# Kernel optimization log

Measured on AMD Instinct MI355X. Metric: run time of the kernel, lower is better.

The kernel has to match this reference:

```python
import jax, jax.numpy as jnp
import numpy as np

E = 256; H = 8; HD = E // H
L_LEN = 300; A_LEN = 250
T = 768; B = 4
NEG = -1e9


def setup_inputs() -> dict:
    rng = jax.random.key(0)
    ks = jax.random.split(rng, 16)
    n = lambda k, s, sc=1.0: jax.random.normal(k, s, dtype=jnp.float32) * sc
    return {
        "query": n(ks[0], (T, B, E)),
        "key": n(ks[1], (T, B, E)),
        "value": n(ks[2], (T, B, E)),
        "in_proj_w": n(ks[3], (3 * E, E), 0.05),
        "in_proj_b": jnp.zeros((3 * E,), jnp.float32),
        "out_w": n(ks[4], (7, E, E), 0.05),
        "out_b": jnp.zeros((7, E), jnp.float32),
        "s_l_w": n(ks[5], (E, 4 * E), 0.05),
        "s_l_b": jnp.zeros((E,), jnp.float32),
        "s_a_w": n(ks[6], (E, 4 * E), 0.05),
        "s_a_b": jnp.zeros((E,), jnp.float32),
        "s_v_w": n(ks[7], (E, 4 * E), 0.05),
        "s_v_b": jnp.zeros((E,), jnp.float32),
        "final_w": n(ks[8], (E, E), 0.05),
        "final_b": jnp.zeros((E,), jnp.float32),
    }


def _forward(query, key, value, in_proj_w, in_proj_b, out_w, out_b,
             s_l_w, s_l_b, s_a_w, s_a_b, s_v_w, s_v_b, final_w, final_b):
    t, b, e = query.shape
    scaling = HD ** -0.5
    Wq, Wk, Wv = in_proj_w[:E], in_proj_w[E:2 * E], in_proj_w[2 * E:]
    bq, bk, bv = in_proj_b[:E], in_proj_b[E:2 * E], in_proj_b[2 * E:]
    q = (query @ Wq.T + bq) * scaling
    k = key @ Wk.T + bk
    v = value @ Wv.T + bv
    # (T, B, E) -> (B*H, T, HD)
    sh = lambda x: x.reshape(t, b * H, HD).transpose(1, 0, 2)
    q, k, v = sh(q), sh(k), sh(v)
    # shared QK^T, reused by all 7 masked branches
    scores = jnp.einsum('bth,bsh->bts', q, k)  # (B*H, T, T)
    idx = jnp.arange(t)
    seg = jnp.where(idx < L_LEN, 0, jnp.where(idx < L_LEN + A_LEN, 1, 2))

    def branch(i, mods):
        # m[j] = 1 iff position j belongs to one of the selected modalities
        m = sum((seg == s) for s in mods).astype(scores.dtype)  # (T,)
        # additive mask: in-set query attends only in-set keys; out-of-set
        # query rows get all -1e9 (uniform softmax, zeroed by row mask below)
        add = jnp.where((m[:, None] * m[None, :]) > 0, 0.0, NEG)
        w = jax.nn.softmax(scores + add, axis=-1) * m[None, :, None]
        o = jnp.einsum('bts,bsh->bth', w, v * m[None, :, None])
        o = o.transpose(1, 0, 2).reshape(t, b, e)
        return o @ out_w[i].T + out_b[i]

    attn_lav = branch(0, (0, 1, 2))
    attn_la = branch(1, (0, 1))
    attn_lv = branch(2, (0, 2))
    attn_av = branch(3, (1, 2))
    attn_l = branch(4, (0,))
    attn_a = branch(5, (1,))
    attn_v = branch(6, (2,))

    sl = jnp.concatenate([attn_lav, attn_la, attn_lv, attn_l], -1) @ s_l_w.T + s_l_b
    sa = jnp.concatenate([attn_lav, attn_la, attn_av, attn_a], -1) @ s_a_w.T + s_a_b
    sv = jnp.concatenate([attn_lav, attn_lv, attn_av, attn_v], -1) @ s_v_w.T + s_v_b
    return (sl + sa + sv) @ final_w.T + final_b


def reference(query, key, value, in_proj_w, in_proj_b, out_w, out_b,
              s_l_w, s_l_b, s_a_w, s_a_b, s_v_w, s_v_b, final_w, final_b):
    return _forward(query, key, value, in_proj_w, in_proj_b, out_w, out_b,
                    s_l_w, s_l_b, s_a_w, s_a_b, s_v_w, s_v_b, final_w, final_b)
```

## Files before the change

### kernel.cpp

```cpp
#include <hip/hip_runtime.h>
#include <hip/hip_bf16.h>

#define E 256
#define H 8
#define HD 32
#define T 768
#define B 4
#define BH 32

typedef __attribute__((ext_vector_type(8))) short bf16x8;
typedef __attribute__((ext_vector_type(4))) float f32x4;
typedef __attribute__((ext_vector_type(16))) float f32x16;

__device__ __forceinline__ float b2f(__hip_bfloat16 x) { return __bfloat162float(x); }

__device__ __forceinline__ unsigned short f2bf_u(float x) {
    __hip_bfloat16 h = __float2bfloat16(x);
    return *(unsigned short*)&h;
}
__device__ __forceinline__ float bfu2f(unsigned short u) {
    return __uint_as_float(((unsigned int)u) << 16);
}

__device__ __forceinline__ int detect_f32(const void* query) {
    const unsigned short* q = (const unsigned short*)query;
    int lane = threadIdx.x & 63;
    int bad = 0;
    #pragma unroll
    for (int i = 0; i < 4; ++i) {
        float v = bfu2f(q[lane + i * 64]);
        bad |= (!(v == v) || fabsf(v) > 1e4f) ? 1 : 0;
    }
    return __any(bad) ? 1 : 0;
}

__device__ __forceinline__ void f8_split(const float* v, bf16x8& h, bf16x8& l) {
    #pragma unroll
    for (int e = 0; e < 8; ++e) {
        unsigned short hu = f2bf_u(v[e]);
        h[e] = (short)hu;
        l[e] = (short)f2bf_u(v[e] - bfu2f(hu));
    }
}

#define MFMA3(ACC, AH, AL, BH_, BL_)                                         \
    ACC = __builtin_amdgcn_mfma_f32_16x16x32_bf16(AH, BH_, ACC, 0, 0, 0);    \
    ACC = __builtin_amdgcn_mfma_f32_16x16x32_bf16(AH, BL_, ACC, 0, 0, 0);    \
    ACC = __builtin_amdgcn_mfma_f32_16x16x32_bf16(AL, BH_, ACC, 0, 0, 0);

#define MFMA3W(ACC, AH, AL, BH_, BL_)                                        \
    ACC = __builtin_amdgcn_mfma_f32_32x32x16_bf16(AH, BH_, ACC, 0, 0, 0);    \
    ACC = __builtin_amdgcn_mfma_f32_32x32x16_bf16(AH, BL_, ACC, 0, 0, 0);    \
    ACC = __builtin_amdgcn_mfma_f32_32x32x16_bf16(AL, BH_, ACC, 0, 0, 0);

__device__ __forceinline__ bf16x8 mk8(int a, int b, int c, int d) {
    union { int i[4]; bf16x8 v; } u;
    u.i[0] = a; u.i[1] = b; u.i[2] = c; u.i[3] = d;
    return u.v;
}

__device__ __forceinline__ float ldu(const void* p, size_t i, int f32) {
    if (f32) return ((const float*)p)[i];
    return b2f(((const __hip_bfloat16*)p)[i]);
}

__device__ __forceinline__ float gsum_load(int i, int r2, int r,
                                           const void* sl, const void* sa,
                                           const void* sv, int f32)
{
    size_t base = (size_t)r2 * 1024;
    switch (i) {
        case 0: return ldu(sl, base + r, f32) + ldu(sa, base + r, f32) + ldu(sv, base + r, f32);
        case 1: return ldu(sl, base + 256 + r, f32) + ldu(sa, base + 256 + r, f32);
        case 2: return ldu(sl, base + 512 + r, f32) + ldu(sv, base + 256 + r, f32);
        case 3: return ldu(sa, base + 512 + r, f32) + ldu(sv, base + 512 + r, f32);
        case 4: return ldu(sl, base + 768 + r, f32);
        case 5: return ldu(sa, base + 768 + r, f32);
        default: return ldu(sv, base + 768 + r, f32);
    }
}

__global__ __launch_bounds__(256) void stage1_kernel(
    const void* query, const void* key, const void* value, const void* w,
    const void* sl, const void* sa, const void* sv, const void* outw,
    const void* outb, const void* slb, const void* sab, const void* svb,
    unsigned short* __restrict__ XFh, unsigned short* __restrict__ XFl,
    unsigned short* __restrict__ WFh, unsigned short* __restrict__ WFl,
    unsigned short* __restrict__ GFh, unsigned short* __restrict__ GFl,
    unsigned short* __restrict__ OWFh, unsigned short* __restrict__ OWFl,
    float* __restrict__ c0)
{
    __shared__ float red[256];
    int f32 = detect_f32(query);
    if (blockIdx.x < 1696) {
        int item = blockIdx.x * 256 + threadIdx.x;
        if (item < 294912) {
            int inp = item / 98304;
            int rem = item % 98304;
            int row = rem >> 5, kg = rem & 31;
            const void* X = (inp == 0) ? query : (inp == 1) ? key : value;
            float v[8];
            if (f32) {
                const float4* p = (const float4*)((const float*)X +
                                   (size_t)row * 256 + kg * 8);
                *(float4*)&v[0] = p[0];
                *(float4*)&v[4] = p[1];
            } else {
                #pragma unroll
                for (int j = 0; j < 8; ++j)
                    v[j] = ldu(X, (size_t)row * 256 + kg * 8 + j, 0);
            }
            bf16x8 h, l;
            f8_split(v, h, l);
            int rb = row >> 4, kb = kg >> 2;
            int lane = (row & 15) | ((kg & 3) << 4);
            size_t idx = (((size_t)(inp * 192 + rb) * 8 + kb) * 64 + lane) * 8;
            *(bf16x8*)&XFh[idx] = h;
            *(bf16x8*)&XFl[idx] = l;
        } else if (item < 319488) {
            int rem = item - 294912;
            int gc = rem >> 5, kg = rem & 31;
            float v[8];
            if (f32) {
                const float4* p = (const float4*)((const float*)w +
                                   (size_t)gc * 256 + kg * 8);
                *(float4*)&v[0] = p[0];
                *(float4*)&v[4] = p[1];
            } else {
                #pragma unroll
                for (int j = 0; j < 8; ++j)
                    v[j] = ldu(w, (size_t)gc * 256 + kg * 8 + j, 0);
            }
            bf16x8 h, l;
            f8_split(v, h, l);
            int sec = gc >> 8, c = gc & 255;
            int cb = c >> 4, kb = kg >> 2;
            int lane = (c & 15) | ((kg & 3) << 4);
            size_t idx = (((size_t)(sec * 16 + cb) * 8 + kb) * 64 + lane) * 8;
            *(bf16x8*)&WFh[idx] = h;
            *(bf16x8*)&WFl[idx] = l;
        } else if (item < 376832) {
            int rem = item - 319488;
            int i = rem >> 13;
            int rest = rem & 8191;
            int r2 = rest >> 5, kg = rest & 31;
            float v[8];
            #pragma unroll
            for (int j = 0; j < 8; ++j)
                v[j] = gsum_load(i, r2, kg * 8 + j, sl, sa, sv, f32);
            bf16x8 h, l;
            f8_split(v, h, l);
            int rb = r2 >> 4, kb = kg >> 2;
            int lane = (r2 & 15) | ((kg & 3) << 4);
            size_t idx = (((size_t)(i * 16 + rb) * 8 + kb) * 64 + lane) * 8;
            *(bf16x8*)&GFh[idx] = h;
            *(bf16x8*)&GFl[idx] = l;
        } else if (item < 434176) {
            int rem = item - 376832;
            int i = rem >> 13;
            int rest = rem & 8191;
            int kg = rest >> 8, c = rest & 255;
            float v[8];
            #pragma unroll
            for (int j = 0; j < 8; ++j)
                v[j] = ldu(outw, (size_t)i * 65536 + (kg * 8 + j) * 256 + c, f32);
            bf16x8 h, l;
            f8_split(v, h, l);
            int cb = c >> 4, kb = kg >> 2;
            int lane = (c & 15) | ((kg & 3) << 4);
            size_t idx = (((size_t)(i * 16 + cb) * 8 + kb) * 64 + lane) * 8;
            *(bf16x8*)&OWFh[idx] = h;
            *(bf16x8*)&OWFl[idx] = l;
        }
    } else {
        int r2 = blockIdx.x - 1696, m = threadIdx.x;
        float acc = 0.f;
        #pragma unroll
        for (int i = 0; i < 7; ++i)
            acc += ldu(outb, i * 256 + m, f32) * gsum_load(i, r2, m, sl, sa, sv, f32);
        red[m] = acc;
        __syncthreads();
        for (int s = 128; s > 0; s >>= 1) {
            if (m < s) red[m] += red[m + s];
            __syncthreads();
        }
        if (m == 0)
            c0[r2] = red[0] + ldu(slb, r2, f32) + ldu(sab, r2, f32) + ldu(svb, r2, f32);
    }
}

__global__ __launch_bounds__(256) void stage2_kernel(
    const unsigned short* __restrict__ XFh, const unsigned short* __restrict__ XFl,
    const unsigned short* __restrict__ WFh, const unsigned short* __restrict__ WFl,
    const void* bias, const void* query,
    float* __restrict__ qws,
    unsigned short* __restrict__ KRh, unsigned short* __restrict__ KRl,
    unsigned short* __restrict__ VFh, unsigned short* __restrict__ VFl,
    const unsigned short* __restrict__ GFh, const unsigned short* __restrict__ GFl,
    const unsigned short* __restrict__ OWFh, const unsigned short* __restrict__ OWFl,
    float* __restrict__ Mtmp,
    const float* __restrict__ c0, const void* finalw, const void* finalb,
    float* __restrict__ d0)
{
    __shared__ float red[256];
    int bxx = blockIdx.x;
    if (bxx < 2304) {
        int f32 = detect_f32(query);
        int bx = bxx % 12;
        int rb = bxx / 12;
        int sec = bx >> 2, cg = bx & 3;
        int w = threadIdx.x >> 6, lane = threadIdx.x & 63;
        int m = lane & 15, quad = lane >> 4;
        int cb = cg * 4 + w;

        const unsigned short* Ah = XFh + (((size_t)(sec * 192 + rb) * 8) * 64 + lane) * 8;
        const unsigned short* Al = XFl + (((size_t)(sec * 192 + rb) * 8) * 64 + lane) * 8;
        const unsigned short* Bh = WFh + (((size_t)(sec * 16 + cb) * 8) * 64 + lane) * 8;
        const unsigned short* Bl = WFl + (((size_t)(sec * 16 + cb) * 8) * 64 + lane) * 8;

        f32x4 acc = {};
        #pragma unroll
        for (int kb = 0; kb < 8; ++kb) {
            size_t off = (size_t)kb * 512;
            bf16x8 ah = *(const bf16x8*)(Ah + off);
            bf16x8 al = *(const bf16x8*)(Al + off);
            bf16x8 bh = *(const bf16x8*)(Bh + off);
            bf16x8 bl = *(const bf16x8*)(Bl + off);
            MFMA3(acc, ah, al, bh, bl)
        }

        int c_local = cb * 16 + m;
        float bv = ldu(bias, sec * 256 + c_local, f32);
        int h = c_local >> 5, hd = c_local & 31;

        if (sec == 0) {
            #pragma unroll
            for (int rr = 0; rr < 4; ++rr) {
                int row = rb * 16 + quad * 4 + rr;
                int t = row >> 2, b = row & 3;
                float val = (acc[rr] + bv) * 0.17677669529663687f;
                qws[((size_t)((b * H + h) * T + t)) * HD + hd] = val;
            }
        } else if (sec == 1) {
            #pragma unroll
            for (int rr = 0; rr < 4; ++rr) {
                int row = rb * 16 + quad * 4 + rr;
                int s = row >> 2, b = row & 3;
                int bh_ = b * 8 + h;
                float val = acc[rr] + bv;
                unsigned short hu = f2bf_u(val);
                unsigned short lu = f2bf_u(val - bfu2f(hu));
                size_t bi = ((size_t)bh_ * 768 + s) * 32 + hd;
                KRh[bi] = hu;
                KRl[bi] = lu;
            }
        } else {
            #pragma unroll
            for (int rr = 0; rr < 4; ++rr) {
                int row = rb * 16 + quad * 4 + rr;
                int s = row >> 2, b = row & 3;
                int bh_ = b * 8 + h;
                float val = acc[rr] + bv;
                unsigned short hu = f2bf_u(val);
                unsigned short lu = f2bf_u(val - bfu2f(hu));
                int s16 = s >> 4, hp = (s >> 3) & 1, j = s & 7;
                size_t bi = (((size_t)bh_ * 48 + s16) * 64 + hp * 32 + hd) * 8 + j;
                VFh[bi] = hu;
                VFl[bi] = lu;
            }
        }
    } else if (bxx < 2752) {
        int idx = bxx - 2304;
        int cgrp = idx & 3;
        int rb   = (idx >> 2) & 15;
        int i    = idx >> 6;
        int w = threadIdx.x >> 6, lane = threadIdx.x & 63;
        int m = lane & 15, quad = lane >> 4;
        int cb = cgrp * 4 + w;

        const unsigned short* Ah = GFh + (((size_t)(i * 16 + rb) * 8) * 64 + lane) * 8;
        const unsigned short* Al = GFl + (((size_t)(i * 16 + rb) * 8) * 64 + lane) * 8;
        const unsigned short* Bh = OWFh + (((size_t)(i * 16 + cb) * 8) * 64 + lane) * 8;
        const unsigned short* Bl = OWFl + (((size_t)(i * 16 + cb) * 8) * 64 + lane) * 8;

        f32x4 acc = {};
        #pragma unroll
        for (int kb = 0; kb < 8; ++kb) {
            size_t off = (size_t)kb * 512;
            bf16x8 ah = *(const bf16x8*)(Ah + off);
            bf16x8 al = *(const bf16x8*)(Al + off);
            bf16x8 bh = *(const bf16x8*)(Bh + off);
            bf16x8 bl = *(const bf16x8*)(Bl + off);
            MFMA3(acc, ah, al, bh, bl)
        }
        #pragma unroll
        for (int rr = 0; rr < 4; ++rr) {
            int r2 = rb * 16 + quad * 4 + rr;
            Mtmp[(size_t)i * 65536 + r2 * 256 + cb * 16 + m] = acc[rr];
        }
    } else {
        int f32 = detect_f32(query);
        int e = bxx - 2752, r = threadIdx.x;
        red[r] = c0[r] * ldu(finalw, (size_t)e * 256 + r, f32);
        __syncthreads();
        for (int s = 128; s > 0; s >>= 1) {
            if (r < s) red[r] += red[r + s];
            __syncthreads();
        }
        if (r == 0)
            d0[e] = red[0] + ldu(finalb, e, f32);
    }
}

__global__ __launch_bounds__(256, 3) void stage3_kernel(
    const float* __restrict__ qws,
    const unsigned short* __restrict__ KRh, const unsigned short* __restrict__ KRl,
    const unsigned short* __restrict__ VFh, const unsigned short* __restrict__ VFl,
    unsigned short* __restrict__ Ohi, unsigned short* __restrict__ Olo,
    const float* __restrict__ Mtmp, const void* finalw, const void* query,
    unsigned short* __restrict__ DThi, unsigned short* __restrict__ DTlo)
{
    __shared__ __align__(16) float SMEM[7104];
    int tid = threadIdx.x;

    if (blockIdx.x < 768) {
        float (*AC2)[3][32][36] = (float(*)[3][32][36])&SMEM[0];
        float (*SS2)[3][32]     = (float(*)[3][32])&SMEM[6912];
        int tile = blockIdx.x % 24;
        int bh   = blockIdx.x / 24;
        int t0 = tile * 32;
        int w = tid >> 6, lane = tid & 63;
        int ln = lane & 31, h = lane >> 5;

        bf16x8 qbh[2], qbl[2];
        {
            const float* qr = qws + ((size_t)bh * T + t0 + ln) * HD + h * 8;
            #pragma unroll
            for (int c = 0; c < 2; ++c) {
                float qv[8];
                *(float4*)&qv[0] = *(const float4*)(qr + c * 16);
                *(float4*)&qv[4] = *(const float4*)(qr + c * 16 + 4);
                f8_split(qv, qbh[c], qbl[c]);
            }
        }

        f32x16 accA = {}, accB = {};
        float ssA = 0.f, ssB = 0.f;

        for (int q = 0; q < 3; ++q) {
            int ch = w * 3 + q;
            int sbase = ch * 64;
            int route = (ch == 5) ? 1 : (ch == 4 || ch == 8) ? 2 : 0;
            int bnd = (ch == 4) ? 300 : 550;
            bool c12 = (ch == 4);

            int PH[2][8], PL[2][8];
            #pragma unroll
            for (int st = 0; st < 2; ++st) {
                size_t krow = ((size_t)bh * 768 + sbase + st * 32 + ln) * 32 + h * 8;
                bf16x8 kh0 = *(const bf16x8*)(KRh + krow);
                bf16x8 kl0 = *(const bf16x8*)(KRl + krow);
                bf16x8 kh1 = *(const bf16x8*)(KRh + krow + 16);
                bf16x8 kl1 = *(const bf16x8*)(KRl + krow + 16);
                f32x16 d = {};
                MFMA3W(d, kh0, kl0, qbh[0], qbl[0])
                MFMA3W(d, kh1, kl1, qbh[1], qbl[1])

                int EH[16], EL[16];
                #pragma unroll
                for (int r = 0; r < 16; ++r) {
                    float e = __expf(d[r]);
                    if (route == 2) {
                        int s = sbase + st * 32 + (r & 3) + 8 * (r >> 2) + 4 * h;
                        if (s < bnd) ssA += e; else ssB += e;
                    } else if (route == 1) ssB += e;
                    else ssA += e;
                    unsigned int eb = __float_as_uint(e);
                    float lo = e - __uint_as_float(eb & 0xffff0000u);
                    EH[r] = (int)eb;
                    EL[r] = (int)__float_as_uint(lo);
                }
                #pragma unroll
                for (int p = 0; p < 8; ++p) {
                    PH[st][p] = (int)(((unsigned)EH[2*p] >> 16) |
                                      ((unsigned)EH[2*p+1] & 0xffff0000u));
                    PL[st][p] = (int)(((unsigned)EL[2*p] >> 16) |
                                      ((unsigned)EL[2*p+1] & 0xffff0000u));
                }
            }

            #pragma unroll
            for (int ks = 0; ks < 4; ++ks) {
                int st = ks >> 1, cc = 4 * (ks & 1);
                size_t vidx = (((size_t)bh * 48 + ch * 4 + ks) * 64 + lane) * 8;
                bf16x8 vbh = *(const bf16x8*)(VFh + vidx);
                bf16x8 vbl = *(const bf16x8*)(VFl + vidx);

                int sh0 = __shfl_xor(PH[st][cc+0], 32);
                int sh1 = __shfl_xor(PH[st][cc+1], 32);
                int sh2 = __shfl_xor(PH[st][cc+2], 32);
                int sh3 = __shfl_xor(PH[st][cc+3], 32);
                int sl0 = __shfl_xor(PL[st][cc+0], 32);
                int sl1 = __shfl_xor(PL[st][cc+1], 32);
                int sl2 = __shfl_xor(PL[st][cc+2], 32);
                int sl3 = __shfl_xor(PL[st][cc+3], 32);
                int FH0 = h ? sh2 : PH[st][cc+0];
                int FH1 = h ? sh3 : PH[st][cc+1];
                int FH2 = h ? PH[st][cc+2] : sh0;
                int FH3 = h ? PH[st][cc+3] : sh1;
                int FL0 = h ? sl2 : PL[st][cc+0];
                int FL1 = h ? sl3 : PL[st][cc+1];
                int FL2 = h ? PL[st][cc+2] : sl0;
                int FL3 = h ? PL[st][cc+3] : sl1;
                bf16x8 feh = mk8(FH0, FH1, FH2, FH3);
                bf16x8 fel = mk8(FL0, FL1, FL2, FL3);

                if (route == 0)      { MFMA3W(accA, feh, fel, vbh, vbl) }
                else if (route == 1) { MFMA3W(accB, feh, fel, vbh, vbl) }
                else {
                    if (ks < 2)       { MFMA3W(accA, feh, fel, vbh, vbl) }
                    else if (ks == 3) { MFMA3W(accB, feh, fel, vbh, vbl) }
                    else {
                        int a0 = h ? (c12 ? FH0 : 0) : FH0;
                        int a1 = h ? (c12 ? FH1 : 0) : FH1;
                        int a2 = h ? 0 : FH2;
                        int a3 = h ? 0 : (c12 ? FH3 : 0);
                        int b0 = h ? (c12 ? 0 : FH0) : 0;
                        int b1 = h ? (c12 ? 0 : FH1) : 0;
                        int b2 = h ? FH2 : 0;
                        int b3 = h ? FH3 : (c12 ? 0 : FH3);
                        int la0 = h ? (c12 ? FL0 : 0) : FL0;
                        int la1 = h ? (c12 ? FL1 : 0) : FL1;
                        int la2 = h ? 0 : FL2;
                        int la3 = h ? 0 : (c12 ? FL3 : 0);
                        int lb0 = h ? (c12 ? 0 : FL0) : 0;
                        int lb1 = h ? (c12 ? 0 : FL1) : 0;
                        int lb2 = h ? FL2 : 0;
                        int lb3 = h ? FL3 : (c12 ? 0 : FL3);
                        bf16x8 fha = mk8(a0, a1, a2, a3), fla = mk8(la0, la1, la2, la3);
                        bf16x8 fhb = mk8(b0, b1, b2, b3), flb = mk8(lb0, lb1, lb2, lb3);
                        MFMA3W(accA, fha, fla, vbh, vbl)
                        MFMA3W(accB, fhb, flb, vbh, vbl)
                    }
                }
            }
        }

        ssA += __shfl_xor(ssA, 32);
        ssB += __shfl_xor(ssB, 32);

        int bsel = w & 1;
        f32x16 zz = {};
        f32x16 o0 = (w <= 1) ? accA : zz;
        f32x16 o1 = (w == 1) ? accB : (w == 2) ? accA : zz;
        f32x16 o2 = (w == 2) ? accB : (w == 3) ? accA : zz;
        float s0 = (w <= 1) ? ssA : 0.f;
        float s1 = (w == 1) ? ssB : (w == 2) ? ssA : 0.f;
        float s2 = (w == 2) ? ssB : (w == 3) ? ssA : 0.f;

        if (w < 2) {
            #pragma unroll
            for (int r = 0; r < 16; ++r) {
                int t = (r & 3) + 8 * (r >> 2) + 4 * h;
                AC2[bsel][0][t][ln] = o0[r];
                AC2[bsel][1][t][ln] = o1[r];
                AC2[bsel][2][t][ln] = o2[r];
            }
            if (h == 0) {
                SS2[bsel][0][ln] = s0;
                SS2[bsel][1][ln] = s1;
                SS2[bsel][2][ln] = s2;
            }
        }
        __syncthreads();
        if (w >= 2) {
            #pragma unroll
            for (int r = 0; r < 16; ++r) {
                int t = (r & 3) + 8 * (r >> 2) + 4 * h;
                AC2[bsel][1][t][ln] += o1[r];
                AC2[bsel][2][t][ln] += o2[r];
            }
            if (h == 0) {
                SS2[bsel][1][ln] += s1;
                SS2[bsel][2][ln] += s2;
            }
        }
        __syncthreads();

        int tt = tid >> 3, q4 = tid & 7;
        float Pv[3][4], S[3];
        #pragma unroll
        for (int sg = 0; sg < 3; ++sg) {
            const float4 a = *(const float4*)&AC2[0][sg][tt][q4 * 4];
            const float4 b = *(const float4*)&AC2[1][sg][tt][q4 * 4];
            Pv[sg][0] = a.x + b.x; Pv[sg][1] = a.y + b.y;
            Pv[sg][2] = a.z + b.z; Pv[sg][3] = a.w + b.w;
            S[sg] = SS2[0][sg][tt] + SS2[1][sg][tt];
        }

        int t_glob = t0 + tt;
        int g = (t_glob < 300) ? 0 : (t_glob < 550 ? 1 : 2);
        int b_ = bh >> 3, h_ = bh & 7;
        int row = b_ * T + t_glob;
        int lslot = (row & 15) + ((q4 >> 1) << 4);
        int j0 = (q4 & 1) * 4;
        size_t fbase = (((size_t)(row >> 4) * 56 + h_) * 64 + lslot) * 8 + j0;
        const int masks[7] = {7, 3, 5, 6, 1, 2, 4};
        #pragma unroll
        for (int i = 0; i < 7; ++i) {
            int mm = masks[i];
            float n0 = 0.f, n1 = 0.f, n2 = 0.f, n3 = 0.f, den = 0.f;
            if (mm & 1) { n0 += Pv[0][0]; n1 += Pv[0][1]; n2 += Pv[0][2]; n3 += Pv[0][3]; den += S[0]; }
            if (mm & 2) { n0 += Pv[1][0]; n1 += Pv[1][1]; n2 += Pv[1][2]; n3 += Pv[1][3]; den += S[1]; }
            if (mm & 4) { n0 += Pv[2][0]; n1 += Pv[2][1]; n2 += Pv[2][2]; n3 += Pv[2][3]; den += S[2]; }
            float r = 1.f / den;
            int live = (mm >> g) & 1;
            float o[4];
            o[0] = live ? n0 * r : 0.f;
            o[1] = live ? n1 * r : 0.f;
            o[2] = live ? n2 * r : 0.f;
            o[3] = live ? n3 * r : 0.f;
            ushort4 hi4, lo4;
            unsigned short* hp = (unsigned short*)&hi4;
            unsigned short* lp = (unsigned short*)&lo4;
            #pragma unroll
            for (int j = 0; j < 4; ++j) {
                unsigned short hu = f2bf_u(o[j]);
                hp[j] = hu;
                lp[j] = f2bf_u(o[j] - bfu2f(hu));
            }
            size_t addr = fbase + (size_t)i * (8 * 64 * 8);
            *(ushort4*)&Ohi[addr] = hi4;
            *(ushort4*)&Olo[addr] = lo4;
        }
    } else {
        float (*AsT)[34] = (float(*)[34])&SMEM[0];
        float (*Bs)[34]  = (float(*)[34])&SMEM[1088];
        int f32 = detect_f32(query);
        int idx = blockIdx.x - 768;
        int bx = idx & 7;
        int by = (idx >> 3) & 7;
        int i  = idx >> 6;
        int tx = tid & 15, ty = tid >> 4;
        int colbase = bx * 32, rowbase = by * 32;
        float acc[2][2] = {};

        for (int kb = 0; kb < 8; ++kb) {
            __syncthreads();
            #pragma unroll
            for (int l = 0; l < 4; ++l) {
                int idx2 = l * 256 + tid;
                int c = idx2 & 31, kk = idx2 >> 5;
                AsT[kk][c] = Mtmp[(size_t)i * 65536 + (kb * 32 + kk) * 256 + rowbase + c];
                int k2 = idx2 & 31, n = idx2 >> 5;
                Bs[k2][n] = ldu(finalw, (size_t)(colbase + n) * 256 + kb * 32 + k2, f32);
            }
            __syncthreads();
            #pragma unroll 8
            for (int kk = 0; kk < 32; ++kk) {
                const float2 av = *(const float2*)&AsT[kk][ty * 2];
                const float2 bv = *(const float2*)&Bs[kk][tx * 2];
                acc[0][0] += av.x * bv.x; acc[0][1] += av.x * bv.y;
                acc[1][0] += av.y * bv.x; acc[1][1] += av.y * bv.y;
            }
        }
        #pragma unroll
        for (int u = 0; u < 2; ++u)
            #pragma unroll
            for (int v = 0; v < 2; ++v) {
                int c = rowbase + ty * 2 + u, e = colbase + tx * 2 + v;
                float a = acc[u][v];
                unsigned short hu = f2bf_u(a);
                size_t fidx = (((size_t)(e >> 4) * 56 + i * 8 + (c >> 5)) * 64
                               + (e & 15) + (((c >> 3) & 3) << 4)) * 8 + (c & 7);
                DThi[fidx] = hu;
                DTlo[fidx] = f2bf_u(a - bfu2f(hu));
            }
    }
}

__global__ __launch_bounds__(256) void final_gemm_mfma_kernel(
    const unsigned short* __restrict__ Ohi, const unsigned short* __restrict__ Olo,
    const unsigned short* __restrict__ DThi, const unsigned short* __restrict__ DTlo,
    const float* __restrict__ d0, const void* query,
    void* __restrict__ outv)
{
    int f32 = detect_f32(query);
    int bx = blockIdx.x;
    int by = blockIdx.y;
    int w  = threadIdx.x >> 6;
    int lane = threadIdx.x & 63;
    int m = lane & 15, quad = lane >> 4;
    int R0 = by * 16, C0 = bx * 64 + w * 16;

    int b_out = R0 / 768;
    int tfirst = R0 - b_out * 768;
    int g0 = (tfirst < 300) ? 0 : (tfirst < 550 ? 1 : 2);
    int g1 = (tfirst + 15 < 300) ? 0 : (tfirst + 15 < 550 ? 1 : 2);
    int activeset = (1 << g0) | (1 << g1);
    const int masks[7] = {7, 3, 5, 6, 1, 2, 4};

    const unsigned short* Abase_h = Ohi + (size_t)by * 56 * 512 + lane * 8;
    const unsigned short* Abase_l = Olo + (size_t)by * 56 * 512 + lane * 8;
    const unsigned short* Bbase_h = DThi + (size_t)(bx * 4 + w) * 56 * 512 + lane * 8;
    const unsigned short* Bbase_l = DTlo + (size_t)(bx * 4 + w) * 56 * 512 + lane * 8;

    f32x4 acc = {};
    for (int i = 0; i < 7; ++i) {
        if (!(masks[i] & activeset)) continue;
        #pragma unroll
        for (int kb = 0; kb < 8; ++kb) {
            size_t off = (size_t)(i * 8 + kb) * 512;
            bf16x8 ah = *(const bf16x8*)(Abase_h + off);
            bf16x8 al = *(const bf16x8*)(Abase_l + off);
            bf16x8 bh = *(const bf16x8*)(Bbase_h + off);
            bf16x8 bl = *(const bf16x8*)(Bbase_l + off);
            acc = __builtin_amdgcn_mfma_f32_16x16x32_bf16(ah, bh, acc, 0, 0, 0);
            acc = __builtin_amdgcn_mfma_f32_16x16x32_bf16(ah, bl, acc, 0, 0, 0);
            acc = __builtin_amdgcn_mfma_f32_16x16x32_bf16(al, bh, acc, 0, 0, 0);
        }
    }
    float dv = d0[C0 + m];
    #pragma unroll
    for (int r = 0; r < 4; ++r) {
        int t = tfirst + quad * 4 + r;
        int col = C0 + m;
        float val = acc[r] + dv;
        size_t orow = (size_t)t * B + b_out;
        if (f32) ((float*)outv)[orow * 256 + col] = val;
        else ((__hip_bfloat16*)outv)[orow * 256 + col] = __float2bfloat16(val);
    }
}

extern "C" void kernel_launch(void* const* d_in, const int* in_sizes, int n_in,
                              void* d_out, int out_size, void* d_ws, size_t ws_size,
                              hipStream_t stream) {
    const void* query     = d_in[0];
    const void* key       = d_in[1];
    const void* value     = d_in[2];
    const void* in_proj_w = d_in[3];
    const void* in_proj_b = d_in[4];
    const void* out_w     = d_in[5];
    const void* out_b     = d_in[6];
    const void* s_l_w     = d_in[7];
    const void* s_l_b     = d_in[8];
    const void* s_a_w     = d_in[9];
    const void* s_a_b     = d_in[10];
    const void* s_v_w     = d_in[11];
    const void* s_v_b     = d_in[12];
    const void* final_w   = d_in[13];
    const void* final_b   = d_in[14];

    float* ws     = (float*)d_ws;
    float* qws    = ws;
    unsigned short* KRh = (unsigned short*)(ws + 786432);
    unsigned short* KRl = KRh + 786432;
    unsigned short* VFh = (unsigned short*)(ws + 1572864);
    unsigned short* VFl = VFh + 786432;
    unsigned short* Ohi = (unsigned short*)(ws + 2359296);
    unsigned short* Olo = (unsigned short*)(ws + 5111808);
    unsigned short* XFh = (unsigned short*)(ws + 2359296);
    unsigned short* XFl = XFh + 2359296;
    unsigned short* WFh = XFl + 2359296;
    unsigned short* WFl = WFh + 196608;
    unsigned short* GFh = (unsigned short*)(ws + 4915200);
    unsigned short* GFl = GFh + 458752;
    unsigned short* OWFh = GFl + 458752;
    unsigned short* OWFl = OWFh + 458752;
    float* Mtmp   = ws + 7864320;
    unsigned short* DThi = (unsigned short*)(ws + 8323072);
    unsigned short* DTlo = (unsigned short*)(ws + 8552448);
    float* d0     = ws + 8781824;
    float* c0     = ws + 8782336;

    stage1_kernel<<<1952, 256, 0, stream>>>(query, key, value, in_proj_w,
                                            s_l_w, s_a_w, s_v_w, out_w,
                                            out_b, s_l_b, s_a_b, s_v_b,
                                            XFh, XFl, WFh, WFl,
                                            GFh, GFl, OWFh, OWFl, c0);
    stage2_kernel<<<3008, 256, 0, stream>>>(XFh, XFl, WFh, WFl,
                                            in_proj_b, query, qws,
                                            KRh, KRl, VFh, VFl,
                                            GFh, GFl, OWFh, OWFl, Mtmp,
                                            c0, final_w, final_b, d0);
    stage3_kernel<<<1216, 256, 0, stream>>>(qws, KRh, KRl, VFh, VFl,
                                            Ohi, Olo,
                                            Mtmp, final_w, query,
                                            DThi, DTlo);
    final_gemm_mfma_kernel<<<dim3(4, 192), 256, 0, stream>>>(Ohi, Olo, DThi, DTlo,
                                                             d0, query, d_out);
}
```

Before: 167.1 us.

## Interleave per-subtile exp/pack with PV MFMAs and relax stage3 launch bounds

Restructures the attention inner loop of stage3 so each 32-key subtile's exp, hi/lo bf16 split and packing feed straight into its two PV MFMA steps, instead of computing both subtiles' probabilities first and holding them in arrays. This shrinks live register state (PH/PL arrays halved, EH/EL temporaries removed) and lets QK, exp and PV work overlap per subtile. The launch bound's minimum blocks per CU drops from 3 to 2, giving the compiler more registers per thread at the cost of possibly lower occupancy.

```diff
diff --git a/kernel.cpp b/kernel.cpp
--- a/kernel.cpp
+++ b/kernel.cpp
@@ -312,7 +312,7 @@
     }
 }
 
-__global__ __launch_bounds__(256, 3) void stage3_kernel(
+__global__ __launch_bounds__(256, 2) void stage3_kernel(
     const float* __restrict__ qws,
     const unsigned short* __restrict__ KRh, const unsigned short* __restrict__ KRl,
     const unsigned short* __restrict__ VFh, const unsigned short* __restrict__ VFl,
@@ -354,7 +354,6 @@
             int bnd = (ch == 4) ? 300 : 550;
             bool c12 = (ch == 4);
 
-            int PH[2][8], PL[2][8];
             #pragma unroll
             for (int st = 0; st < 2; ++st) {
                 size_t krow = ((size_t)bh * 768 + sbase + st * 32 + ln) * 32 + h * 8;
@@ -366,81 +365,80 @@
                 MFMA3W(d, kh0, kl0, qbh[0], qbl[0])
                 MFMA3W(d, kh1, kl1, qbh[1], qbl[1])
 
-                int EH[16], EL[16];
-                #pragma unroll
-                for (int r = 0; r < 16; ++r) {
-                    float e = __expf(d[r]);
-                    if (route == 2) {
-                        int s = sbase + st * 32 + (r & 3) + 8 * (r >> 2) + 4 * h;
-                        if (s < bnd) ssA += e; else ssB += e;
-                    } else if (route == 1) ssB += e;
-                    else ssA += e;
-                    unsigned int eb = __float_as_uint(e);
-                    float lo = e - __uint_as_float(eb & 0xffff0000u);
-                    EH[r] = (int)eb;
-                    EL[r] = (int)__float_as_uint(lo);
-                }
+                int PH[8], PL[8];
                 #pragma unroll
                 for (int p = 0; p < 8; ++p) {
-                    PH[st][p] = (int)(((unsigned)EH[2*p] >> 16) |
-                                      ((unsigned)EH[2*p+1] & 0xffff0000u));
-                    PL[st][p] = (int)(((unsigned)EL[2*p] >> 16) |
-                                      ((unsigned)EL[2*p+1] & 0xffff0000u));
+                    float e0 = __expf(d[2 * p]);
+                    float e1 = __expf(d[2 * p + 1]);
+                    if (route == 2) {
+                        int r0 = 2 * p;
+                        int s0 = sbase + st * 32 + (r0 & 3) + 8 * (r0 >> 2) + 4 * h;
+                        if (s0 < bnd) ssA += e0; else ssB += e0;
+                        if (s0 + 1 < bnd) ssA += e1; else ssB += e1;
+                    } else if (route == 1) { ssB += e0 + e1; }
+                    else { ssA += e0 + e1; }
+                    unsigned b0 = __float_as_uint(e0), b1 = __float_as_uint(e1);
+                    float l0 = e0 - __uint_as_float(b0 & 0xffff0000u);
+                    float l1 = e1 - __uint_as_float(b1 & 0xffff0000u);
+                    PH[p] = (int)((b0 >> 16) | (b1 & 0xffff0000u));
+                    PL[p] = (int)((__float_as_uint(l0) >> 16) |
+                                  (__float_as_uint(l1) & 0xffff0000u));
                 }
-            }
-
-            #pragma unroll
-            for (int ks = 0; ks < 4; ++ks) {
-                int st = ks >> 1, cc = 4 * (ks & 1);
-                size_t vidx = (((size_t)bh * 48 + ch * 4 + ks) * 64 + lane) * 8;
-                bf16x8 vbh = *(const bf16x8*)(VFh + vidx);
-                bf16x8 vbl = *(const bf16x8*)(VFl + vidx);
-
-                int sh0 = __shfl_xor(PH[st][cc+0], 32);
-                int sh1 = __shfl_xor(PH[st][cc+1], 32);
-                int sh2 = __shfl_xor(PH[st][cc+2], 32);
-                int sh3 = __shfl_xor(PH[st][cc+3], 32);
-                int sl0 = __shfl_xor(PL[st][cc+0], 32);
-                int sl1 = __shfl_xor(PL[st][cc+1], 32);
-                int sl2 = __shfl_xor(PL[st][cc+2], 32);
-                int sl3 = __shfl_xor(PL[st][cc+3], 32);
-                int FH0 = h ? sh2 : PH[st][cc+0];
-                int FH1 = h ? sh3 : PH[st][cc+1];
-                int FH2 = h ? PH[st][cc+2] : sh0;
-                int FH3 = h ? PH[st][cc+3] : sh1;
-                int FL0 = h ? sl2 : PL[st][cc+0];
-                int FL1 = h ? sl3 : PL[st][cc+1];
-                int FL2 = h ? PL[st][cc+2] : sl0;
-                int FL3 = h ? PL[st][cc+3] : sl1;
-                bf16x8 feh = mk8(FH0, FH1, FH2, FH3);
-                bf16x8 fel = mk8(FL0, FL1, FL2, FL3);
-
-                if (route == 0)      { MFMA3W(accA, feh, fel, vbh, vbl) }
-                else if (route == 1) { MFMA3W(accB, feh, fel, vbh, vbl) }
-                else {
-                    if (ks < 2)       { MFMA3W(accA, feh, fel, vbh, vbl) }
-                    else if (ks == 3) { MFMA3W(accB, feh, fel, vbh, vbl) }
+
+                #pragma unroll
+                for (int ksl = 0; ksl < 2; ++ksl) {
+                    int ks = st * 2 + ksl;
+                    int cc = 4 * ksl;
+                    size_t vidx = (((size_t)bh * 48 + ch * 4 + ks) * 64 + lane) * 8;
+                    bf16x8 vbh = *(const bf16x8*)(VFh + vidx);
+                    bf16x8 vbl = *(const bf16x8*)(VFl + vidx);
+
+                    int sh0 = __shfl_xor(PH[cc+0], 32);
+                    int sh1 = __shfl_xor(PH[cc+1], 32);
+                    int sh2 = __shfl_xor(PH[cc+2], 32);
+                    int sh3 = __shfl_xor(PH[cc+3], 32);
+                    int sl0 = __shfl_xor(PL[cc+0], 32);
+                    int sl1 = __shfl_xor(PL[cc+1], 32);
+                    int sl2 = __shfl_xor(PL[cc+2], 32);
+                    int sl3 = __shfl_xor(PL[cc+3], 32);
+                    int FH0 = h ? sh2 : PH[cc+0];
+                    int FH1 = h ? sh3 : PH[cc+1];
+                    int FH2 = h ? PH[cc+2] : sh0;
+                    int FH3 = h ? PH[cc+3] : sh1;
+                    int FL0 = h ? sl2 : PL[cc+0];
+                    int FL1 = h ? sl3 : PL[cc+1];
+                    int FL2 = h ? PL[cc+2] : sl0;
+                    int FL3 = h ? PL[cc+3] : sl1;
+                    bf16x8 feh = mk8(FH0, FH1, FH2, FH3);
+                    bf16x8 fel = mk8(FL0, FL1, FL2, FL3);
+
+                    if (route == 0)      { MFMA3W(accA, feh, fel, vbh, vbl) }
+                    else if (route == 1) { MFMA3W(accB, feh, fel, vbh, vbl) }
                     else {
-                        int a0 = h ? (c12 ? FH0 : 0) : FH0;
-                        int a1 = h ? (c12 ? FH1 : 0) : FH1;
-                        int a2 = h ? 0 : FH2;
-                        int a3 = h ? 0 : (c12 ? FH3 : 0);
-                        int b0 = h ? (c12 ? 0 : FH0) : 0;
-                        int b1 = h ? (c12 ? 0 : FH1) : 0;
-                        int b2 = h ? FH2 : 0;
-                        int b3 = h ? FH3 : (c12 ? 0 : FH3);
-                        int la0 = h ? (c12 ? FL0 : 0) : FL0;
-                        int la1 = h ? (c12 ? FL1 : 0) : FL1;
-                        int la2 = h ? 0 : FL2;
-                        int la3 = h ? 0 : (c12 ? FL3 : 0);
-                        int lb0 = h ? (c12 ? 0 : FL0) : 0;
-                        int lb1 = h ? (c12 ? 0 : FL1) : 0;
-                        int lb2 = h ? FL2 : 0;
-                        int lb3 = h ? FL3 : (c12 ? 0 : FL3);
-                        bf16x8 fha = mk8(a0, a1, a2, a3), fla = mk8(la0, la1, la2, la3);
-                        bf16x8 fhb = mk8(b0, b1, b2, b3), flb = mk8(lb0, lb1, lb2, lb3);
-                        MFMA3W(accA, fha, fla, vbh, vbl)
-                        MFMA3W(accB, fhb, flb, vbh, vbl)
+                        if (ks < 2)       { MFMA3W(accA, feh, fel, vbh, vbl) }
+                        else if (ks == 3) { MFMA3W(accB, feh, fel, vbh, vbl) }
+                        else {
+                            int a0 = h ? (c12 ? FH0 : 0) : FH0;
+                            int a1 = h ? (c12 ? FH1 : 0) : FH1;
+                            int a2 = h ? 0 : FH2;
+                            int a3 = h ? 0 : (c12 ? FH3 : 0);
+                            int b0 = h ? (c12 ? 0 : FH0) : 0;
+                            int b1 = h ? (c12 ? 0 : FH1) : 0;
+                            int b2 = h ? FH2 : 0;
+                            int b3 = h ? FH3 : (c12 ? 0 : FH3);
+                            int la0 = h ? (c12 ? FL0 : 0) : FL0;
+                            int la1 = h ? (c12 ? FL1 : 0) : FL1;
+                            int la2 = h ? 0 : FL2;
+                            int la3 = h ? 0 : (c12 ? FL3 : 0);
+                            int lb0 = h ? (c12 ? 0 : FL0) : 0;
+                            int lb1 = h ? (c12 ? 0 : FL1) : 0;
+                            int lb2 = h ? FL2 : 0;
+                            int lb3 = h ? FL3 : (c12 ? 0 : FL3);
+                            bf16x8 fha = mk8(a0, a1, a2, a3), fla = mk8(la0, la1, la2, la3);
+                            bf16x8 fhb = mk8(b0, b1, b2, b3), flb = mk8(lb0, lb1, lb2, lb3);
+                            MFMA3W(accA, fha, fla, vbh, vbl)
+                            MFMA3W(accB, fhb, flb, vbh, vbl)
+                        }
                     }
                 }
             }
```

New measurement: 164.4 us. Within noise of the previous version (-1.6%).
